# Performance work log

Measured on AMD Instinct MI355X. Metric: run time of the kernel, lower is better.

Reference implementation:

```python
import jax, jax.numpy as jnp
import numpy as np

B, N, H, NH = 8, 1024, 768, 12
AS = H // NH
SCALE = AS ** -0.5
NEG_SLOPE = 0.02  # LeakyReLU(0.02)
M = 256           # occurrence pairs per batch item


def _lin(k, out_d, in_d):
    k1, k2 = jax.random.split(k)
    w = jax.random.normal(k1, (out_d, in_d), jnp.float32) * (in_d ** -0.5)
    b = jax.random.normal(k2, (out_d,), jnp.float32) * 0.01
    return w, b


def setup_inputs():
    key = jax.random.key(0)
    ks = jax.random.split(key, 10)
    W_var, b_var = _lin(ks[0], H, H)
    W_sym, b_sym = _lin(ks[1], H, H)
    W_score, b_score = _lin(ks[2], 1, 2 * H)
    W_cross, b_cross = _lin(ks[3], 1, H)
    W_atom, b_atom = _lin(ks[4], H, 2 * H)
    W_q, b_q = _lin(ks[5], H, H)
    W_k, b_k = _lin(ks[6], H, H)
    W_v, b_v = _lin(ks[7], H, H)
    W_o, b_o = _lin(ks[8], H, H)
    x = jax.random.normal(ks[9], (B, N, H), jnp.float32)
    # predicates every 3rd node starting at 2 (no overlapping writes, i+1 < N)
    pp = np.zeros((B, N), np.int32)
    pp[:, 2:N - 2:3] = 1
    rng = np.random.default_rng(0)
    occ = np.stack([rng.permutation(N)[:2 * M].reshape(M, 2) for _ in range(B)]).astype(np.int32)
    return dict(
        x=x,
        atom_graph=jnp.zeros((B, N, N), jnp.float32),
        variable_graph=jnp.zeros((B, N, N), jnp.float32),
        W_var=W_var, b_var=b_var, W_sym=W_sym, b_sym=b_sym,
        W_score=W_score, b_score=b_score, W_cross=W_cross, b_cross=b_cross,
        W_atom=W_atom, b_atom=b_atom, W_q=W_q, b_q=b_q, W_k=W_k, b_k=b_k,
        W_v=W_v, b_v=b_v, W_o=W_o, b_o=b_o,
        predicate_pos=jnp.asarray(pp),
        variable_tags=jnp.zeros((B, N), jnp.int32),
        attention_mask=jnp.ones((B, N), jnp.int32),
        occurrence_list=jnp.asarray(occ),
    )


def reference(x, atom_graph, variable_graph,
              W_var, b_var, W_sym, b_sym, W_score, b_score, W_cross, b_cross,
              W_atom, b_atom, W_q, b_q, W_k, b_k, W_v, b_v, W_o, b_o,
              predicate_pos, variable_tags, attention_mask, occurrence_list):
    lrelu = lambda v: jax.nn.leaky_relu(v, NEG_SLOPE)
    idx = jnp.arange(N)
    pred = predicate_pos == 1                              # [B,N]
    pp_prev2 = jnp.roll(predicate_pos, 2, axis=1)          # pp[i-2]
    # branch: single-neighbor var (i==0 or pp[i-2]==1) vs averaged neighbors
    single = (idx[None, :] == 0) | ((idx[None, :] >= 2) & (pp_prev2 == 1))
    x_prev = jnp.roll(x, 1, axis=1)
    x_next = jnp.roll(x, -1, axis=1)
    var_in = jnp.where(single[..., None], x_next, (x_prev + x_next) * 0.5)
    var_feat = var_in @ W_var.T + b_var
    sym_feat = x @ W_sym.T + b_sym
    t = jnp.tanh(jnp.concatenate([var_feat, sym_feat], axis=-1))
    s = lrelu(t @ W_score.T + b_score)[..., 0]             # [B,N] edge scores
    # write masks: (i-1,i)/(i,i-1) for preds i>=1; (i,i+1)/(i+1,i) for i<=1 or double branch
    lower = pred & (idx[None, :] >= 1)
    upper = pred & ((idx[None, :] <= 1) | ~single)
    sl = jnp.where(lower, s, 0.0)
    su = jnp.where(upper, s, 0.0)
    im1 = jnp.clip(idx - 1, 0, N - 1)
    ip1 = jnp.clip(idx + 1, 0, N - 1)
    AG = atom_graph
    AG = AG.at[:, im1, idx].add(sl).at[:, idx, im1].add(sl)
    AG = AG.at[:, idx, ip1].add(su).at[:, ip1, idx].add(su)
    # variable (cross-atom occurrence) graph
    o0, o1 = occurrence_list[..., 0], occurrence_list[..., 1]
    barange = jnp.arange(B)[:, None]
    xm = (x[barange, o0] + x[barange, o1]) * 0.5           # [B,M,H]
    sc = lrelu(xm @ W_cross.T + b_cross)[..., 0]           # [B,M]
    VG = variable_graph.at[barange, o0, o1].add(sc).at[barange, o1, o0].add(sc)
    # multi-head attention with graph biases
    q = (x @ W_q.T + b_q).reshape(B, N, NH, AS).transpose(0, 2, 1, 3) * SCALE
    k = (x @ W_k.T + b_k).reshape(B, N, NH, AS).transpose(0, 2, 1, 3)
    v = (x @ W_v.T + b_v).reshape(B, N, NH, AS).transpose(0, 2, 1, 3)
    att = jnp.einsum('bhnd,bhmd->bhnm', q, k)
    AG = 0.2 * AG + 0.8 * (AG @ AG)
    VG2 = VG @ VG
    att = att + AG[:, None] + VG2[:, None]
    att = jax.nn.softmax(att, axis=-1)                     # dropout omitted (eval)
    y = jnp.einsum('bhnm,bhmd->bhnd', att, v).transpose(0, 2, 1, 3).reshape(B, N, H)
    y = y @ W_o.T + b_o
    # path embedding: weighted mean of per-predicate atom embeds (weight 2 or 3)
    y_prev = jnp.roll(y, 1, axis=1)
    y_next = jnp.roll(y, -1, axis=1)
    var_y = jnp.where(single[..., None], y_next, (y_prev + y_next) * 0.5)
    atom = jnp.concatenate([var_y, y], axis=-1) @ W_atom.T + b_atom  # [B,N,H]
    triple = upper & (idx[None, :] >= 1)
    w = jnp.where(pred, jnp.where(triple, 3.0, 2.0), 0.0)
    pm = (w[..., None] * atom).sum(axis=1) / w.sum(axis=1)[:, None]  # [B,H]
    return jnp.broadcast_to(pm[:, None, :], (B, N, H))
```

## Files before the change

### kernel.cpp

```cpp
#include <hip/hip_runtime.h>
#include <hip/hip_bf16.h>

#define BB 8
#define NN 1024
#define HH 768
#define NHD 12
#define ASZ 64
#define MM 256
#define QSCALE 0.125f
#define NSLOPE 0.02f
#define LOG2E 1.44269504f
#define PRMAX 384

typedef __attribute__((ext_vector_type(8))) short bf16x8;
typedef __attribute__((ext_vector_type(4))) float f32x4;

#define EXP2F(x) __builtin_amdgcn_exp2f(x)
#define RCPF(x)  __builtin_amdgcn_rcpf(x)

#define OFFB_QB    ((size_t)0)
#define OFFB_KB    ((size_t)12582912)
#define OFFB_VB    ((size_t)25165824)
#define OFFB_XB    ((size_t)37748736)
#define OFFB_WQB   ((size_t)50331648)
#define OFFB_WKB   ((size_t)51511296)
#define OFFB_WVB   ((size_t)52690944)
#define OFFB_WVAR  ((size_t)53870592)
#define OFFB_WSYM  ((size_t)55050240)
#define OFFB_SRAW  ((size_t)56229888)
#define OFFB_DIAG  ((size_t)56262656)
#define OFFB_BIAS4 ((size_t)56295424)
#define OFFB_PLIST ((size_t)56426496)
#define OFFB_PCNT  ((size_t)56459264)
#define OFFB_SUMW  ((size_t)56459296)
#define OFFB_ZZ    ((size_t)56459328)
#define OFFB_TV    ((size_t)56508480)
#define OFFB_PM    ((size_t)56557632)
#define OFFB_VROWS ((size_t)56582208)

__device__ __forceinline__ float lrelu(float v) { return v >= 0.f ? v : NSLOPE * v; }

__device__ __forceinline__ ushort f2bf(float f) {
  return (ushort)((__float_as_uint(f) + 0x8000u) >> 16);
}
__device__ __forceinline__ float bf2f(ushort u) {
  union { unsigned u; float f; } v; v.u = (unsigned)u << 16;
  return v.f;
}
__device__ __forceinline__ unsigned packbf2(float lo, float hi) {
  unsigned a = __float_as_uint(hi) + 0x8000u;
  unsigned b = __float_as_uint(lo) + 0x8000u;
  return __builtin_amdgcn_perm(a, b, 0x07060302u);
}
__device__ __forceinline__ float fast_tanh(float x) {
  float e = EXP2F(x * (2.f * LOG2E));
  return 1.f - 2.f * RCPF(e + 1.f);
}

__device__ __forceinline__ void coefs(const int* ppb, int j, float& c1, float& c2) {
  auto pred = [&](int tt) { return tt >= 0 && tt < NN && ppb[tt] == 1; };
  auto single = [&](int tt) { return tt == 0 || (tt >= 2 && ppb[tt - 2] == 1); };
  auto wgt = [&](int tt) {
    if (!pred(tt)) return 0.f;
    bool tri = (tt >= 1) && (tt <= 1 || !single(tt));
    return tri ? 3.f : 2.f;
  };
  float a = 0.f;
  if (pred(j + 1)) a += wgt(j + 1) * (single(j + 1) ? 0.f : 0.5f);
  if (j >= 1 && pred(j - 1)) a += wgt(j - 1) * (single(j - 1) ? 1.f : 0.5f);
  c1 = a;
  c2 = wgt(j);
}

__global__ void k_pred(const int* __restrict__ pp, int* __restrict__ plist,
                       int* __restrict__ pcnt, float* __restrict__ sumw,
                       float* __restrict__ sraw, float* __restrict__ diag,
                       float* __restrict__ zz) {
  int b = blockIdx.x;
  int lane = threadIdx.x;
  const int* ppb = pp + b * NN;
  int base = 0;
  float wacc = 0.f;
  for (int c = 0; c < NN; c += 64) {
    int i = c + lane;
    bool isp = ppb[i] == 1;
    unsigned long long mask = __ballot(isp);
    if (isp) {
      int pos = base + __popcll(mask & ((1ull << lane) - 1ull));
      plist[b * NN + pos] = i;
      bool sing = (i == 0) || (i >= 2 && ppb[i - 2] == 1);
      bool tri = (i >= 1) && (i <= 1 || !sing);
      wacc += tri ? 3.f : 2.f;
    }
    base += __popcll(mask);
  }
  for (int off = 32; off; off >>= 1) wacc += __shfl_xor(wacc, off);
  if (lane == 0) { pcnt[b] = base; sumw[b] = wacc; }
  for (int c = lane; c < NN; c += 64) { sraw[b * NN + c] = 0.f; diag[b * NN + c] = 0.f; }
  for (int c = lane; c < HH; c += 64) {
    zz[b * HH + c] = 0.f;
    zz[BB * HH + b * HH + c] = 0.f;
  }
}

#define NXQ (BB * NN * HH / 4)
#define WQ  (HH * HH / 4)
#define NCVT ((NXQ + 5 * WQ) / 256)
__global__ void k_cvtall(const float* __restrict__ x,
                         const float* __restrict__ s1, const float* __restrict__ s2,
                         const float* __restrict__ s3, const float* __restrict__ s4,
                         const float* __restrict__ s5,
                         ushort* __restrict__ dx,
                         ushort* __restrict__ d1, ushort* __restrict__ d2,
                         ushort* __restrict__ d3, ushort* __restrict__ d4,
                         ushort* __restrict__ d5,
                         const int* __restrict__ occ, const float* __restrict__ Wc,
                         const float* __restrict__ bc, float* __restrict__ diag) {
  if (blockIdx.x < NCVT) {
    int idx = blockIdx.x * 256 + threadIdx.x;
    const float* src; ushort* dst; int off;
    if (idx < NXQ) { src = x; dst = dx; off = idx; }
    else {
      int r = idx - NXQ;
      int z = r / WQ;
      off = r - z * WQ;
      src = z == 0 ? s1 : z == 1 ? s2 : z == 2 ? s3 : z == 3 ? s4 : s5;
      dst = z == 0 ? d1 : z == 1 ? d2 : z == 2 ? d3 : z == 3 ? d4 : d5;
    }
    float4 v = ((const float4*)src)[off];
    ushort4 o;
    o.x = f2bf(v.x); o.y = f2bf(v.y); o.z = f2bf(v.z); o.w = f2bf(v.w);
    ((ushort4*)dst)[off] = o;
  } else {
    int g = (blockIdx.x - NCVT) * 4 + (threadIdx.x >> 6);
    int lane = threadIdx.x & 63;
    int b = g >> 8, m = g & (MM - 1);
    int o0 = occ[(b * MM + m) * 2 + 0];
    int o1 = occ[(b * MM + m) * 2 + 1];
    const float* x0 = x + (size_t)(b * NN + o0) * HH;
    const float* x1 = x + (size_t)(b * NN + o1) * HH;
    float acc = 0.f;
    for (int d = lane; d < HH; d += 64) acc += 0.5f * (x0[d] + x1[d]) * Wc[d];
    for (int off = 32; off; off >>= 1) acc += __shfl_xor(acc, off);
    if (lane == 0) {
      float sc = lrelu(acc + bc[0]);
      float sq = sc * sc;
      diag[b * NN + o0] = sq;
      diag[b * NN + o1] = sq;
    }
  }
}

__global__ void k_gather(const ushort* __restrict__ xb, const int* __restrict__ pp,
                         const int* __restrict__ plist, const int* __restrict__ pcnt,
                         ushort* __restrict__ vrows) {
  int b = blockIdx.y;
  int j = blockIdx.x * 4 + (threadIdx.x >> 6);
  int lane = threadIdx.x & 63;
  if (j >= pcnt[b]) return;
  int i = plist[b * NN + j];
  bool sing = (i == 0) || (i >= 2 && pp[b * NN + i - 2] == 1);
  float wa = sing ? 0.f : 0.5f, wb = sing ? 1.f : 0.5f;
  const ushort* rp = xb + (size_t)(b * NN + ((i - 1) & (NN - 1))) * HH;
  const ushort* rn = xb + (size_t)(b * NN + ((i + 1) & (NN - 1))) * HH;
  ushort* dst = vrows + ((size_t)b * PRMAX + j) * HH;
#pragma unroll
  for (int it = 0; it < 3; ++it) {
    int d4 = lane + it * 64;
    ushort4 p4 = ((const ushort4*)rp)[d4];
    ushort4 n4 = ((const ushort4*)rn)[d4];
    ushort4 o;
    o.x = f2bf(wa * bf2f(p4.x) + wb * bf2f(n4.x));
    o.y = f2bf(wa * bf2f(p4.y) + wb * bf2f(n4.y));
    o.z = f2bf(wa * bf2f(p4.z) + wb * bf2f(n4.z));
    o.w = f2bf(wa * bf2f(p4.w) + wb * bf2f(n4.w));
    ((ushort4*)dst)[d4] = o;
  }
}

__global__ void k_bias(const int* __restrict__ pp, const float* __restrict__ s_raw,
                       const float* __restrict__ diag, const float* __restrict__ b_score,
                       float4* __restrict__ bias4) {
  int g = blockIdx.x * 256 + threadIdx.x;
  int b = g >> 10, r = g & (NN - 1);
  const int* ppb = pp + b * NN;
  int i = -1;
  if (ppb[r] == 1) i = r;
  else if (r + 1 < NN && ppb[r + 1] == 1) i = r + 1;
  else if (r >= 1 && ppb[r - 1] == 1) i = r - 1;
  float v0 = 0.f, v1 = 0.f, v2 = 0.f; int cw = r;
  if (i >= 1 && i + 1 < NN) {
    float s = lrelu(s_raw[b * NN + i] + b_score[0]);
    float s2 = s * s;
    cw = i - 1;
    if (i == r) { v0 = 0.2f * s; v1 = 1.6f * s2; v2 = 0.2f * s; }
    else       { v0 = 0.8f * s2; v1 = 0.2f * s; v2 = 0.8f * s2; }
  }
  int slot = r - cw;
  float d = diag[g];
  if (slot == 0) v0 += d; else if (slot == 1) v1 += d; else v2 += d;
  bias4[g] = make_float4(__int_as_float(cw), v0 * LOG2E, v1 * LOG2E, v2 * LOG2E);
}

#define GEMM_BLKS 1152
__global__ __launch_bounds__(256, 3) void k_mats(
    const ushort* __restrict__ X, const ushort* __restrict__ vrows,
    const int* __restrict__ plist, const int* __restrict__ pcnt,
    const ushort* __restrict__ Wvar, const ushort* __restrict__ Wsym,
    const float* __restrict__ bvar, const float* __restrict__ bsym,
    const float* __restrict__ wscore, float* __restrict__ s_raw,
    const ushort* __restrict__ W0, const ushort* __restrict__ W1, const ushort* __restrict__ W2,
    const float* __restrict__ b0, const float* __restrict__ b1, const float* __restrict__ b2,
    ushort* __restrict__ C0, ushort* __restrict__ C1, ushort* __restrict__ C2) {
  __shared__ ushort Sm[16384];
  __shared__ int pl[64];
  __shared__ float red[64];
  const int t = threadIdx.x;
  const int w = t >> 6, lane = t & 63, lg = lane >> 4, lm = lane & 15;
  const int r0 = t >> 3, c = t & 7;
  const int ssw = (c ^ (r0 & 7)) * 8;
  if (blockIdx.x < GEMM_BLKS) {
    const int z = blockIdx.x / 384;
    const int r = blockIdx.x % 384;
    const int m0 = (r & 63) * 128, n0 = (r >> 6) * 128;
    const ushort* W = z == 0 ? W0 : (z == 1 ? W1 : W2);
    const float* bias = z == 0 ? b0 : (z == 1 ? b1 : b2);
    ushort* C = z == 0 ? C0 : (z == 1 ? C1 : C2);
    const float alpha = z == 0 ? QSCALE * LOG2E : 1.f;
    ushort* As = Sm;
    ushort* Bs = Sm + 8192;
    const int wm = (w >> 1) * 64, wn = (w & 1) * 64;
    const ushort* Xp = X + (size_t)(m0 + r0) * HH + c * 8;
    const ushort* Wp = W + (size_t)(n0 + r0) * HH + c * 8;
    uint4 xa0 = *(const uint4*)Xp;
    uint4 xa1 = *(const uint4*)(Xp + (size_t)32 * HH);
    uint4 xa2 = *(const uint4*)(Xp + (size_t)64 * HH);
    uint4 xa3 = *(const uint4*)(Xp + (size_t)96 * HH);
    uint4 wb0 = *(const uint4*)Wp;
    uint4 wb1 = *(const uint4*)(Wp + (size_t)32 * HH);
    uint4 wb2 = *(const uint4*)(Wp + (size_t)64 * HH);
    uint4 wb3 = *(const uint4*)(Wp + (size_t)96 * HH);
    f32x4 acc[4][4] = {};
    for (int k0 = 0; k0 < HH; k0 += 64) {
      if (k0) __syncthreads();
      *(uint4*)&As[r0 * 64 + ssw] = xa0;
      *(uint4*)&As[(r0 + 32) * 64 + ssw] = xa1;
      *(uint4*)&As[(r0 + 64) * 64 + ssw] = xa2;
      *(uint4*)&As[(r0 + 96) * 64 + ssw] = xa3;
      *(uint4*)&Bs[r0 * 64 + ssw] = wb0;
      *(uint4*)&Bs[(r0 + 32) * 64 + ssw] = wb1;
      *(uint4*)&Bs[(r0 + 64) * 64 + ssw] = wb2;
      *(uint4*)&Bs[(r0 + 96) * 64 + ssw] = wb3;
      __syncthreads();
      if (k0 + 64 < HH) {
        Xp += 64; Wp += 64;
        xa0 = *(const uint4*)Xp;
        xa1 = *(const uint4*)(Xp + (size_t)32 * HH);
        xa2 = *(const uint4*)(Xp + (size_t)64 * HH);
        xa3 = *(const uint4*)(Xp + (size_t)96 * HH);
        wb0 = *(const uint4*)Wp;
        wb1 = *(const uint4*)(Wp + (size_t)32 * HH);
        wb2 = *(const uint4*)(Wp + (size_t)64 * HH);
        wb3 = *(const uint4*)(Wp + (size_t)96 * HH);
      }
      bf16x8 af[4][2], bfr[4][2];
#pragma unroll
      for (int mt = 0; mt < 4; ++mt)
#pragma unroll
        for (int kt = 0; kt < 2; ++kt) {
          int row = wm + mt * 16 + lm, ch = lg + kt * 4;
          af[mt][kt] = *(bf16x8*)&As[row * 64 + ((ch ^ (row & 7)) * 8)];
        }
#pragma unroll
      for (int nt = 0; nt < 4; ++nt)
#pragma unroll
        for (int kt = 0; kt < 2; ++kt) {
          int row = wn + nt * 16 + lm, ch = lg + kt * 4;
          bfr[nt][kt] = *(bf16x8*)&Bs[row * 64 + ((ch ^ (row & 7)) * 8)];
        }
#pragma unroll
      for (int mt = 0; mt < 4; ++mt)
#pragma unroll
        for (int nt = 0; nt < 4; ++nt)
#pragma unroll
          for (int kt = 0; kt < 2; ++kt)
            acc[mt][nt] = __builtin_amdgcn_mfma_f32_16x16x32_bf16(af[mt][kt], bfr[nt][kt], acc[mt][nt], 0, 0, 0);
    }
    if (z == 2) {
#pragma unroll
      for (int nt = 0; nt < 4; ++nt) {
        int col = n0 + wn + nt * 16 + lm;
        int hh = col >> 6, dd = col & 63;
        float bcol = bias[col];
#pragma unroll
        for (int mt = 0; mt < 4; ++mt) {
          int row0 = m0 + wm + mt * 16 + lg * 4;
          int bb2 = row0 >> 10, nr = row0 & (NN - 1);
          ushort4 o;
          o.x = f2bf(acc[mt][nt][0] + bcol);
          o.y = f2bf(acc[mt][nt][1] + bcol);
          o.z = f2bf(acc[mt][nt][2] + bcol);
          o.w = f2bf(acc[mt][nt][3] + bcol);
          *(ushort4*)(C + ((size_t)(bb2 * NHD + hh) * ASZ + dd) * NN + nr) = o;
        }
      }
    } else {
#pragma unroll
      for (int nt = 0; nt < 4; ++nt) {
        int col = n0 + wn + nt * 16 + lm;
        float bcol = bias[col];
#pragma unroll
        for (int mt = 0; mt < 4; ++mt)
#pragma unroll
          for (int rr = 0; rr < 4; ++rr) {
            int row = m0 + wm + mt * 16 + lg * 4 + rr;
            C[(size_t)row * HH + col] = f2bf((acc[mt][nt][rr] + bcol) * alpha);
          }
      }
    }
  } else {
    const int bid2 = blockIdx.x - GEMM_BLKS;
    const int b = bid2 / 72;
    const int rem = bid2 % 72;
    const int j0 = (rem / 12) * 64;
    const int n0g = (rem % 12) * 128;
    const int cnt = pcnt[b];
    if (j0 >= cnt) return;
    const bool symh = n0g >= HH;
    const int n0 = symh ? n0g - HH : n0g;
    const ushort* W = symh ? Wsym : Wvar;
    const float* bias = symh ? bsym : bvar;
    ushort* As = Sm;
    ushort* Bs = Sm + 4096;
    const int wm = (w >> 1) * 32, wn = (w & 1) * 64;
    if (t < 64) {
      int j = j0 + t;
      pl[t] = (j < cnt) ? plist[b * NN + j] : 2;
      red[t] = 0.f;
    }
    __syncthreads();
    const ushort* ap0; const ushort* ap1;
    if (symh) {
      const ushort* xbb = X + (size_t)b * NN * HH;
      ap0 = xbb + (size_t)pl[r0] * HH + c * 8;
      ap1 = xbb + (size_t)pl[r0 + 32] * HH + c * 8;
    } else {
      const ushort* vrb = vrows + ((size_t)b * PRMAX + j0) * HH;
      ap0 = vrb + (size_t)r0 * HH + c * 8;
      ap1 = vrb + (size_t)(r0 + 32) * HH + c * 8;
    }
    const ushort* bp = W + (size_t)(n0 + r0) * HH + c * 8;
    uint4 ar0 = *(const uint4*)ap0;
    uint4 ar1 = *(const uint4*)ap1;
    uint4 br0 = *(const uint4*)bp;
    uint4 br1 = *(const uint4*)(bp + (size_t)32 * HH);
    uint4 br2 = *(const uint4*)(bp + (size_t)64 * HH);
    uint4 br3 = *(const uint4*)(bp + (size_t)96 * HH);
    f32x4 acc[2][4] = {};
    for (int k0 = 0; k0 < HH; k0 += 64) {
      if (k0) __syncthreads();
      *(uint4*)&As[r0 * 64 + ssw] = ar0;
      *(uint4*)&As[(r0 + 32) * 64 + ssw] = ar1;
      *(uint4*)&Bs[r0 * 64 + ssw] = br0;
      *(uint4*)&Bs[(r0 + 32) * 64 + ssw] = br1;
      *(uint4*)&Bs[(r0 + 64) * 64 + ssw] = br2;
      *(uint4*)&Bs[(r0 + 96) * 64 + ssw] = br3;
      __syncthreads();
      if (k0 + 64 < HH) {
        ap0 += 64; ap1 += 64; bp += 64;
        ar0 = *(const uint4*)ap0;
        ar1 = *(const uint4*)ap1;
        br0 = *(const uint4*)bp;
        br1 = *(const uint4*)(bp + (size_t)32 * HH);
        br2 = *(const uint4*)(bp + (size_t)64 * HH);
        br3 = *(const uint4*)(bp + (size_t)96 * HH);
      }
      bf16x8 af[2][2], bfr[4][2];
#pragma unroll
      for (int mt = 0; mt < 2; ++mt)
#pragma unroll
        for (int kt = 0; kt < 2; ++kt) {
          int row = wm + mt * 16 + lm, ch = lg + kt * 4;
          af[mt][kt] = *(bf16x8*)&As[row * 64 + ((ch ^ (row & 7)) * 8)];
        }
#pragma unroll
      for (int nt = 0; nt < 4; ++nt)
#pragma unroll
        for (int kt = 0; kt < 2; ++kt) {
          int row = wn + nt * 16 + lm, ch = lg + kt * 4;
          bfr[nt][kt] = *(bf16x8*)&Bs[row * 64 + ((ch ^ (row & 7)) * 8)];
        }
#pragma unroll
      for (int mt = 0; mt < 2; ++mt)
#pragma unroll
        for (int nt = 0; nt < 4; ++nt)
#pragma unroll
          for (int kt = 0; kt < 2; ++kt)
            acc[mt][nt] = __builtin_amdgcn_mfma_f32_16x16x32_bf16(af[mt][kt], bfr[nt][kt], acc[mt][nt], 0, 0, 0);
    }
    float bcol[4], wcol[4];
#pragma unroll
    for (int nt = 0; nt < 4; ++nt) {
      int cl = wn + nt * 16 + lm;
      bcol[nt] = bias[n0 + cl];
      wcol[nt] = wscore[n0g + cl];
    }
#pragma unroll
    for (int mt = 0; mt < 2; ++mt)
#pragma unroll
      for (int rr = 0; rr < 4; ++rr) {
        float p = 0.f;
#pragma unroll
        for (int nt = 0; nt < 4; ++nt)
          p += fast_tanh(acc[mt][nt][rr] + bcol[nt]) * wcol[nt];
        p += __shfl_xor(p, 1); p += __shfl_xor(p, 2);
        p += __shfl_xor(p, 4); p += __shfl_xor(p, 8);
        if (lm == 0) atomicAdd(&red[wm + mt * 16 + lg * 4 + rr], p);
      }
    __syncthreads();
    if (t < 64) {
      int j2 = j0 + t;
      if (j2 < cnt) atomicAdd(&s_raw[b * NN + pl[t]], red[t]);
    }
  }
}

__global__ __launch_bounds__(256, 6) void k_attn2(
    const ushort* __restrict__ qg, const ushort* __restrict__ kg, const ushort* __restrict__ vtg,
    const float4* __restrict__ bias4, const int* __restrict__ pp, float* __restrict__ zz) {
  __shared__ ushort Ks[64 * 64];
  __shared__ ushort Vts[64 * 64];
  const int rb = blockIdx.y, h = blockIdx.x >> 3, b = blockIdx.x & 7;
  const int n0 = rb * 64;
  const int t = threadIdx.x, w = t >> 6, lane = t & 63, lg = lane >> 4, lm = lane & 15;
  const int qbase = n0 + w * 16;
  const ushort* qrow = qg + (size_t)(b * NN + qbase + lm) * HH + h * ASZ;
  bf16x8 qf[2];
  qf[0] = *(const bf16x8*)(qrow + lg * 8);
  qf[1] = *(const bf16x8*)(qrow + lg * 8 + 32);
  float4 bz = bias4[b * NN + qbase + lm];
  const int cwq = __float_as_int(bz.x);
  f32x4 suml = {0.f, 0.f, 0.f, 0.f};
  f32x4 y[4] = {};
  const ushort* kb = kg + (size_t)(b * NN) * HH + h * ASZ;
  const ushort* vtb = vtg + (size_t)(b * NHD + h) * ASZ * NN;
  const int srow = t >> 3, sc = t & 7;
  const int arow = (srow & 35) | ((srow & 4) << 2) | ((srow & 24) >> 1);
  const int kssw = (sc ^ (arow & 7)) * 8;
  const int vssw = (sc ^ (srow & 7)) * 8;
  const ushort* kptr = kb + (size_t)srow * HH + sc * 8;
  const ushort* vptr = vtb + (size_t)srow * NN + sc * 8;
  uint4 ka = *(const uint4*)kptr;
  uint4 kc = *(const uint4*)(kptr + (size_t)32 * HH);
  uint4 va = *(const uint4*)vptr;
  uint4 vb2 = *(const uint4*)(vptr + (size_t)32 * NN);
  for (int tile = 0; tile < 16; ++tile) {
    const int c0 = tile * 64;
    *(uint4*)&Ks[arow * 64 + kssw] = ka;
    *(uint4*)&Ks[(arow + 32) * 64 + kssw] = kc;
    *(uint4*)&Vts[srow * 64 + vssw] = va;
    *(uint4*)&Vts[(srow + 32) * 64 + vssw] = vb2;
    __syncthreads();
    if (tile < 15) {
      kptr += (size_t)64 * HH; vptr += 64;
      ka = *(const uint4*)kptr;
      kc = *(const uint4*)(kptr + (size_t)32 * HH);
      va = *(const uint4*)vptr;
      vb2 = *(const uint4*)(vptr + (size_t)32 * NN);
    }
    f32x4 s[4] = {};
    __builtin_amdgcn_s_setprio(1);
#pragma unroll
    for (int nt = 0; nt < 4; ++nt) {
      int krow = lm + nt * 16, sw = krow & 7;
#pragma unroll
      for (int kt = 0; kt < 2; ++kt) {
        bf16x8 kf = *(bf16x8*)&Ks[krow * 64 + (((lg + kt * 4) ^ sw) * 8)];
        s[nt] = __builtin_amdgcn_mfma_f32_16x16x32_bf16(kf, qf[kt], s[nt], 0, 0, 0);
      }
    }
    __builtin_amdgcn_s_setprio(0);
    if (c0 <= qbase + 17 && qbase <= c0 + 65) {
#pragma unroll
      for (int nt = 0; nt < 4; ++nt) {
        int kb2 = c0 + (nt >> 1) * 32 + lg * 8 + (nt & 1) * 4;
#pragma unroll
        for (int r = 0; r < 4; ++r) {
          int dd = kb2 + r - cwq;
          if (dd >= 0 && dd < 3) s[nt][r] += (dd == 0) ? bz.y : (dd == 1 ? bz.z : bz.w);
        }
      }
    }
#pragma unroll
    for (int nt = 0; nt < 4; ++nt)
#pragma unroll
      for (int e = 0; e < 4; ++e) {
        float p = EXP2F(s[nt][e]);
        s[nt][e] = p;
        suml[e] += p;
      }
    union { unsigned u[4]; bf16x8 v; } pk[2];
#pragma unroll
    for (int kt = 0; kt < 2; ++kt) {
      pk[kt].u[0] = packbf2(s[2 * kt][0], s[2 * kt][1]);
      pk[kt].u[1] = packbf2(s[2 * kt][2], s[2 * kt][3]);
      pk[kt].u[2] = packbf2(s[2 * kt + 1][0], s[2 * kt + 1][1]);
      pk[kt].u[3] = packbf2(s[2 * kt + 1][2], s[2 * kt + 1][3]);
    }
    __builtin_amdgcn_s_setprio(1);
#pragma unroll
    for (int nt = 0; nt < 4; ++nt) {
      int vrow = lm + nt * 16, sw = vrow & 7;
#pragma unroll
      for (int kt = 0; kt < 2; ++kt) {
        bf16x8 vf = *(bf16x8*)&Vts[vrow * 64 + (((lg + kt * 4) ^ sw) * 8)];
        y[nt] = __builtin_amdgcn_mfma_f32_16x16x32_bf16(pk[kt].v, vf, y[nt], 0, 0, 0);
      }
    }
    __builtin_amdgcn_s_setprio(0);
    __syncthreads();
  }
  float ts = (suml[0] + suml[1]) + (suml[2] + suml[3]);
  ts += __shfl_xor(ts, 16);
  ts += __shfl_xor(ts, 32);
  float invl = 1.f / ts;
  float invq[4], c1v[4], c2v[4];
#pragma unroll
  for (int r = 0; r < 4; ++r) {
    invq[r] = __shfl(invl, lg * 4 + r);
    coefs(pp + b * NN, qbase + lg * 4 + r, c1v[r], c2v[r]);
  }
  float a1[4], a2[4];
#pragma unroll
  for (int nt = 0; nt < 4; ++nt) {
    float u1 = 0.f, u2 = 0.f;
#pragma unroll
    for (int r = 0; r < 4; ++r) {
      float yv = y[nt][r] * invq[r];
      u1 += c1v[r] * yv;
      u2 += c2v[r] * yv;
    }
    u1 += __shfl_xor(u1, 16); u1 += __shfl_xor(u1, 32);
    u2 += __shfl_xor(u2, 16); u2 += __shfl_xor(u2, 32);
    a1[nt] = u1; a2[nt] = u2;
  }
  if (lg == 0) {
#pragma unroll
    for (int nt = 0; nt < 4; ++nt) {
      atomicAdd(&zz[b * HH + h * ASZ + nt * 16 + lm], a1[nt]);
      atomicAdd(&zz[BB * HH + b * HH + h * ASZ + nt * 16 + lm], a2[nt]);
    }
  }
}

__global__ void k_f1(const float* __restrict__ Wo, const float* __restrict__ bo,
                     const float* __restrict__ zz, const float* __restrict__ sumw,
                     float* __restrict__ tvec) {
  int b = blockIdx.y;
  int w = threadIdx.x >> 6, lane = threadIdx.x & 63;
  float inv = 1.f / sumw[b];
  const float* z1 = zz + b * HH;
  const float* z2 = zz + BB * HH + b * HH;
  float zr1[12], zr2[12];
#pragma unroll
  for (int m = 0; m < 12; ++m) { zr1[m] = z1[lane + 64 * m] * inv; zr2[m] = z2[lane + 64 * m] * inv; }
  for (int j = 0; j < 8; ++j) {
    int o = blockIdx.x * 32 + w * 8 + j;
    const float* wrow = Wo + (size_t)o * HH;
    float a1 = 0.f, a2 = 0.f;
#pragma unroll
    for (int m = 0; m < 12; ++m) { float wv = wrow[lane + 64 * m]; a1 += wv * zr1[m]; a2 += wv * zr2[m]; }
    for (int mask = 32; mask; mask >>= 1) { a1 += __shfl_xor(a1, mask); a2 += __shfl_xor(a2, mask); }
    if (lane == 0) { tvec[b * HH + o] = a1 + bo[o]; tvec[BB * HH + b * HH + o] = a2 + bo[o]; }
  }
}

__global__ void k_f2(const float* __restrict__ Wa, const float* __restrict__ ba,
                     const float* __restrict__ tvec, float* __restrict__ pm) {
  int b = blockIdx.y;
  int w = threadIdx.x >> 6, lane = threadIdx.x & 63;
  const float* t1 = tvec + b * HH;
  const float* t2 = tvec + BB * HH + b * HH;
  float r1[12], r2[12];
#pragma unroll
  for (int m = 0; m < 12; ++m) { r1[m] = t1[lane + 64 * m]; r2[m] = t2[lane + 64 * m]; }
  for (int j = 0; j < 8; ++j) {
    int o = blockIdx.x * 32 + w * 8 + j;
    const float* wrow = Wa + (size_t)o * (2 * HH);
    float a = 0.f;
#pragma unroll
    for (int m = 0; m < 12; ++m) a += wrow[lane + 64 * m] * r1[m];
#pragma unroll
    for (int m = 0; m < 12; ++m) a += wrow[HH + lane + 64 * m] * r2[m];
    for (int mask = 32; mask; mask >>= 1) a += __shfl_xor(a, mask);
    if (lane == 0) pm[b * HH + o] = a + ba[o];
  }
}

__global__ void k_bcast(const float* __restrict__ pm, float* __restrict__ out) {
  size_t g = (size_t)blockIdx.x * 256 + threadIdx.x;
  int b = (int)(g / ((size_t)NN * HH / 4));
  int hh4 = (int)(g % (HH / 4));
  float4 val = *(const float4*)(pm + b * HH + hh4 * 4);
  *(float4*)(out + g * 4) = val;
}

extern "C" void kernel_launch(void* const* d_in, const int* in_sizes, int n_in,
                              void* d_out, int out_size, void* d_ws, size_t ws_size,
                              hipStream_t stream) {
  (void)in_sizes; (void)n_in; (void)out_size; (void)ws_size;
  const float* x       = (const float*)d_in[0];
  const float* W_var   = (const float*)d_in[3];
  const float* b_var   = (const float*)d_in[4];
  const float* W_sym   = (const float*)d_in[5];
  const float* b_sym   = (const float*)d_in[6];
  const float* W_score = (const float*)d_in[7];
  const float* b_score = (const float*)d_in[8];
  const float* W_cross = (const float*)d_in[9];
  const float* b_cross = (const float*)d_in[10];
  const float* W_atom  = (const float*)d_in[11];
  const float* b_atom  = (const float*)d_in[12];
  const float* W_q     = (const float*)d_in[13];
  const float* b_q     = (const float*)d_in[14];
  const float* W_k     = (const float*)d_in[15];
  const float* b_k     = (const float*)d_in[16];
  const float* W_v     = (const float*)d_in[17];
  const float* b_v     = (const float*)d_in[18];
  const float* W_o     = (const float*)d_in[19];
  const float* b_o     = (const float*)d_in[20];
  const int*   pp      = (const int*)d_in[21];
  const int*   occ     = (const int*)d_in[24];
  float* out = (float*)d_out;
  char* wsb = (char*)d_ws;
  ushort* qb  = (ushort*)(wsb + OFFB_QB);
  ushort* kbf = (ushort*)(wsb + OFFB_KB);
  ushort* vtb = (ushort*)(wsb + OFFB_VB);
  ushort* xb  = (ushort*)(wsb + OFFB_XB);
  ushort* wqb = (ushort*)(wsb + OFFB_WQB);
  ushort* wkb = (ushort*)(wsb + OFFB_WKB);
  ushort* wvb = (ushort*)(wsb + OFFB_WVB);
  ushort* wvar = (ushort*)(wsb + OFFB_WVAR);
  ushort* wsym = (ushort*)(wsb + OFFB_WSYM);
  ushort* vrows = (ushort*)(wsb + OFFB_VROWS);
  float* sraw = (float*)(wsb + OFFB_SRAW);
  float* diag = (float*)(wsb + OFFB_DIAG);
  float4* bias4 = (float4*)(wsb + OFFB_BIAS4);
  int* plist = (int*)(wsb + OFFB_PLIST);
  int* pcnt  = (int*)(wsb + OFFB_PCNT);
  float* sumw = (float*)(wsb + OFFB_SUMW);
  float* zz   = (float*)(wsb + OFFB_ZZ);
  float* tv   = (float*)(wsb + OFFB_TV);
  float* pm   = (float*)(wsb + OFFB_PM);

  k_pred<<<BB, 64, 0, stream>>>(pp, plist, pcnt, sumw, sraw, diag, zz);
  k_cvtall<<<NCVT + BB * MM / 4, 256, 0, stream>>>(
      x, W_q, W_k, W_v, W_var, W_sym, xb, wqb, wkb, wvb, wvar, wsym,
      occ, W_cross, b_cross, diag);
  k_gather<<<dim3(PRMAX / 4, BB), 256, 0, stream>>>(xb, pp, plist, pcnt, vrows);
  k_mats<<<GEMM_BLKS + 576, 256, 0, stream>>>(
      xb, vrows, plist, pcnt, wvar, wsym, b_var, b_sym, W_score, sraw,
      wqb, wkb, wvb, b_q, b_k, b_v, qb, kbf, vtb);
  k_bias<<<BB * NN / 256, 256, 0, stream>>>(pp, sraw, diag, b_score, bias4);
  k_attn2<<<dim3(NHD * BB, NN / 64), 256, 0, stream>>>(qb, kbf, vtb, bias4, pp, zz);
  k_f1<<<dim3(24, BB), 256, 0, stream>>>(W_o, b_o, zz, sumw, tv);
  k_f2<<<dim3(24, BB), 256, 0, stream>>>(W_atom, b_atom, tv, pm);
  k_bcast<<<BB * NN * HH / 1024, 256, 0, stream>>>(pm, out);
}
```

Before: 153.7 us.

## Drop bf16 copy of x; convert on the fly in GEMM loads and fuse gather

The separate fp32→bf16 conversion of the whole x tensor is removed. The QKV and var/sym GEMMs now read fp32 x directly and pack it to bf16 as they stage into shared memory. The gather of neighbour rows is folded into the conversion kernel and reads fp32 x, which removes one launch. A block-index swizzle across the GEMM grid is also added. This saves a full write and read of the converted x, at the cost of doubling the global bytes the GEMM A-operand loads fetch and adding register pressure and conversion ALU work in the inner loop.

```diff
diff --git a/kernel.cpp b/kernel.cpp
--- a/kernel.cpp
+++ b/kernel.cpp
@@ -21,7 +21,6 @@
 #define OFFB_QB    ((size_t)0)
 #define OFFB_KB    ((size_t)12582912)
 #define OFFB_VB    ((size_t)25165824)
-#define OFFB_XB    ((size_t)37748736)
 #define OFFB_WQB   ((size_t)50331648)
 #define OFFB_WKB   ((size_t)51511296)
 #define OFFB_WVB   ((size_t)52690944)
@@ -42,10 +41,6 @@
 
 __device__ __forceinline__ ushort f2bf(float f) {
   return (ushort)((__float_as_uint(f) + 0x8000u) >> 16);
-}
-__device__ __forceinline__ float bf2f(ushort u) {
-  union { unsigned u; float f; } v; v.u = (unsigned)u << 16;
-  return v.f;
 }
 __device__ __forceinline__ unsigned packbf2(float lo, float hi) {
   unsigned a = __float_as_uint(hi) + 0x8000u;
@@ -103,36 +98,33 @@
   }
 }
 
-#define NXQ (BB * NN * HH / 4)
 #define WQ  (HH * HH / 4)
-#define NCVT ((NXQ + 5 * WQ) / 256)
+#define WCVTB (5 * WQ / 256)
+#define CROSSB (BB * MM / 4)
+#define GATB (PRMAX / 4 * BB)
 __global__ void k_cvtall(const float* __restrict__ x,
                          const float* __restrict__ s1, const float* __restrict__ s2,
                          const float* __restrict__ s3, const float* __restrict__ s4,
                          const float* __restrict__ s5,
-                         ushort* __restrict__ dx,
                          ushort* __restrict__ d1, ushort* __restrict__ d2,
                          ushort* __restrict__ d3, ushort* __restrict__ d4,
                          ushort* __restrict__ d5,
                          const int* __restrict__ occ, const float* __restrict__ Wc,
-                         const float* __restrict__ bc, float* __restrict__ diag) {
-  if (blockIdx.x < NCVT) {
+                         const float* __restrict__ bc, float* __restrict__ diag,
+                         const int* __restrict__ pp, const int* __restrict__ plist,
+                         const int* __restrict__ pcnt, ushort* __restrict__ vrows) {
+  if (blockIdx.x < WCVTB) {
     int idx = blockIdx.x * 256 + threadIdx.x;
-    const float* src; ushort* dst; int off;
-    if (idx < NXQ) { src = x; dst = dx; off = idx; }
-    else {
-      int r = idx - NXQ;
-      int z = r / WQ;
-      off = r - z * WQ;
-      src = z == 0 ? s1 : z == 1 ? s2 : z == 2 ? s3 : z == 3 ? s4 : s5;
-      dst = z == 0 ? d1 : z == 1 ? d2 : z == 2 ? d3 : z == 3 ? d4 : d5;
-    }
+    int z = idx / WQ;
+    int off = idx - z * WQ;
+    const float* src = z == 0 ? s1 : z == 1 ? s2 : z == 2 ? s3 : z == 3 ? s4 : s5;
+    ushort* dst = z == 0 ? d1 : z == 1 ? d2 : z == 2 ? d3 : z == 3 ? d4 : d5;
     float4 v = ((const float4*)src)[off];
     ushort4 o;
     o.x = f2bf(v.x); o.y = f2bf(v.y); o.z = f2bf(v.z); o.w = f2bf(v.w);
     ((ushort4*)dst)[off] = o;
-  } else {
-    int g = (blockIdx.x - NCVT) * 4 + (threadIdx.x >> 6);
+  } else if (blockIdx.x < WCVTB + CROSSB) {
+    int g = (blockIdx.x - WCVTB) * 4 + (threadIdx.x >> 6);
     int lane = threadIdx.x & 63;
     int b = g >> 8, m = g & (MM - 1);
     int o0 = occ[(b * MM + m) * 2 + 0];
@@ -148,33 +140,30 @@
       diag[b * NN + o0] = sq;
       diag[b * NN + o1] = sq;
     }
-  }
-}
-
-__global__ void k_gather(const ushort* __restrict__ xb, const int* __restrict__ pp,
-                         const int* __restrict__ plist, const int* __restrict__ pcnt,
-                         ushort* __restrict__ vrows) {
-  int b = blockIdx.y;
-  int j = blockIdx.x * 4 + (threadIdx.x >> 6);
-  int lane = threadIdx.x & 63;
-  if (j >= pcnt[b]) return;
-  int i = plist[b * NN + j];
-  bool sing = (i == 0) || (i >= 2 && pp[b * NN + i - 2] == 1);
-  float wa = sing ? 0.f : 0.5f, wb = sing ? 1.f : 0.5f;
-  const ushort* rp = xb + (size_t)(b * NN + ((i - 1) & (NN - 1))) * HH;
-  const ushort* rn = xb + (size_t)(b * NN + ((i + 1) & (NN - 1))) * HH;
-  ushort* dst = vrows + ((size_t)b * PRMAX + j) * HH;
-#pragma unroll
-  for (int it = 0; it < 3; ++it) {
-    int d4 = lane + it * 64;
-    ushort4 p4 = ((const ushort4*)rp)[d4];
-    ushort4 n4 = ((const ushort4*)rn)[d4];
-    ushort4 o;
-    o.x = f2bf(wa * bf2f(p4.x) + wb * bf2f(n4.x));
-    o.y = f2bf(wa * bf2f(p4.y) + wb * bf2f(n4.y));
-    o.z = f2bf(wa * bf2f(p4.z) + wb * bf2f(n4.z));
-    o.w = f2bf(wa * bf2f(p4.w) + wb * bf2f(n4.w));
-    ((ushort4*)dst)[d4] = o;
+  } else {
+    int g2 = blockIdx.x - (WCVTB + CROSSB);
+    int b = g2 / (PRMAX / 4);
+    int j = (g2 % (PRMAX / 4)) * 4 + (threadIdx.x >> 6);
+    int lane = threadIdx.x & 63;
+    if (j >= pcnt[b]) return;
+    int i = plist[b * NN + j];
+    bool sing = (i == 0) || (i >= 2 && pp[b * NN + i - 2] == 1);
+    float wa = sing ? 0.f : 0.5f, wb = sing ? 1.f : 0.5f;
+    const float* rp = x + (size_t)(b * NN + ((i - 1) & (NN - 1))) * HH;
+    const float* rn = x + (size_t)(b * NN + ((i + 1) & (NN - 1))) * HH;
+    ushort* dst = vrows + ((size_t)b * PRMAX + j) * HH;
+#pragma unroll
+    for (int it = 0; it < 3; ++it) {
+      int d4 = lane + it * 64;
+      float4 p4 = ((const float4*)rp)[d4];
+      float4 n4 = ((const float4*)rn)[d4];
+      ushort4 o;
+      o.x = f2bf(wa * p4.x + wb * n4.x);
+      o.y = f2bf(wa * p4.y + wb * n4.y);
+      o.z = f2bf(wa * p4.z + wb * n4.z);
+      o.w = f2bf(wa * p4.w + wb * n4.w);
+      ((ushort4*)dst)[d4] = o;
+    }
   }
 }
 
@@ -203,8 +192,9 @@
 }
 
 #define GEMM_BLKS 1152
+#define MATS_BLKS 1728
 __global__ __launch_bounds__(256, 3) void k_mats(
-    const ushort* __restrict__ X, const ushort* __restrict__ vrows,
+    const float* __restrict__ xf, const ushort* __restrict__ vrows,
     const int* __restrict__ plist, const int* __restrict__ pcnt,
     const ushort* __restrict__ Wvar, const ushort* __restrict__ Wsym,
     const float* __restrict__ bvar, const float* __restrict__ bsym,
@@ -215,13 +205,14 @@
   __shared__ ushort Sm[16384];
   __shared__ int pl[64];
   __shared__ float red[64];
+  const int bid = (blockIdx.x & 7) * (MATS_BLKS / 8) + (blockIdx.x >> 3);
   const int t = threadIdx.x;
   const int w = t >> 6, lane = t & 63, lg = lane >> 4, lm = lane & 15;
   const int r0 = t >> 3, c = t & 7;
   const int ssw = (c ^ (r0 & 7)) * 8;
-  if (blockIdx.x < GEMM_BLKS) {
-    const int z = blockIdx.x / 384;
-    const int r = blockIdx.x % 384;
+  if (bid < GEMM_BLKS) {
+    const int z = bid / 384;
+    const int r = bid % 384;
     const int m0 = (r & 63) * 128, n0 = (r >> 6) * 128;
     const ushort* W = z == 0 ? W0 : (z == 1 ? W1 : W2);
     const float* bias = z == 0 ? b0 : (z == 1 ? b1 : b2);
@@ -230,38 +221,36 @@
     ushort* As = Sm;
     ushort* Bs = Sm + 8192;
     const int wm = (w >> 1) * 64, wn = (w & 1) * 64;
-    const ushort* Xp = X + (size_t)(m0 + r0) * HH + c * 8;
+    const float* Xp = xf + (size_t)(m0 + r0) * HH + c * 8;
     const ushort* Wp = W + (size_t)(n0 + r0) * HH + c * 8;
-    uint4 xa0 = *(const uint4*)Xp;
-    uint4 xa1 = *(const uint4*)(Xp + (size_t)32 * HH);
-    uint4 xa2 = *(const uint4*)(Xp + (size_t)64 * HH);
-    uint4 xa3 = *(const uint4*)(Xp + (size_t)96 * HH);
-    uint4 wb0 = *(const uint4*)Wp;
-    uint4 wb1 = *(const uint4*)(Wp + (size_t)32 * HH);
-    uint4 wb2 = *(const uint4*)(Wp + (size_t)64 * HH);
-    uint4 wb3 = *(const uint4*)(Wp + (size_t)96 * HH);
+    float4 xaA[4], xaB[4];
+    uint4 wb[4];
+#pragma unroll
+    for (int i = 0; i < 4; ++i) {
+      xaA[i] = *(const float4*)(Xp + (size_t)(i * 32) * HH);
+      xaB[i] = *(const float4*)(Xp + (size_t)(i * 32) * HH + 4);
+      wb[i] = *(const uint4*)(Wp + (size_t)(i * 32) * HH);
+    }
     f32x4 acc[4][4] = {};
     for (int k0 = 0; k0 < HH; k0 += 64) {
       if (k0) __syncthreads();
-      *(uint4*)&As[r0 * 64 + ssw] = xa0;
-      *(uint4*)&As[(r0 + 32) * 64 + ssw] = xa1;
-      *(uint4*)&As[(r0 + 64) * 64 + ssw] = xa2;
-      *(uint4*)&As[(r0 + 96) * 64 + ssw] = xa3;
-      *(uint4*)&Bs[r0 * 64 + ssw] = wb0;
-      *(uint4*)&Bs[(r0 + 32) * 64 + ssw] = wb1;
-      *(uint4*)&Bs[(r0 + 64) * 64 + ssw] = wb2;
-      *(uint4*)&Bs[(r0 + 96) * 64 + ssw] = wb3;
+#pragma unroll
+      for (int i = 0; i < 4; ++i) {
+        uint4 u;
+        u.x = packbf2(xaA[i].x, xaA[i].y); u.y = packbf2(xaA[i].z, xaA[i].w);
+        u.z = packbf2(xaB[i].x, xaB[i].y); u.w = packbf2(xaB[i].z, xaB[i].w);
+        *(uint4*)&As[(r0 + i * 32) * 64 + ssw] = u;
+        *(uint4*)&Bs[(r0 + i * 32) * 64 + ssw] = wb[i];
+      }
       __syncthreads();
       if (k0 + 64 < HH) {
         Xp += 64; Wp += 64;
-        xa0 = *(const uint4*)Xp;
-        xa1 = *(const uint4*)(Xp + (size_t)32 * HH);
-        xa2 = *(const uint4*)(Xp + (size_t)64 * HH);
-        xa3 = *(const uint4*)(Xp + (size_t)96 * HH);
-        wb0 = *(const uint4*)Wp;
-        wb1 = *(const uint4*)(Wp + (size_t)32 * HH);
-        wb2 = *(const uint4*)(Wp + (size_t)64 * HH);
-        wb3 = *(const uint4*)(Wp + (size_t)96 * HH);
+#pragma unroll
+        for (int i = 0; i < 4; ++i) {
+          xaA[i] = *(const float4*)(Xp + (size_t)(i * 32) * HH);
+          xaB[i] = *(const float4*)(Xp + (size_t)(i * 32) * HH + 4);
+          wb[i] = *(const uint4*)(Wp + (size_t)(i * 32) * HH);
+        }
       }
       bf16x8 af[4][2], bfr[4][2];
 #pragma unroll
@@ -319,7 +308,7 @@
       }
     }
   } else {
-    const int bid2 = blockIdx.x - GEMM_BLKS;
+    const int bid2 = bid - GEMM_BLKS;
     const int b = bid2 / 72;
     const int rem = bid2 % 72;
     const int j0 = (rem / 12) * 64;
@@ -339,19 +328,28 @@
       red[t] = 0.f;
     }
     __syncthreads();
-    const ushort* ap0; const ushort* ap1;
+    const float* af0 = nullptr; const float* af1 = nullptr;
+    const ushort* ab0 = nullptr; const ushort* ab1 = nullptr;
     if (symh) {
-      const ushort* xbb = X + (size_t)b * NN * HH;
-      ap0 = xbb + (size_t)pl[r0] * HH + c * 8;
-      ap1 = xbb + (size_t)pl[r0 + 32] * HH + c * 8;
+      const float* xbb = xf + (size_t)b * NN * HH;
+      af0 = xbb + (size_t)pl[r0] * HH + c * 8;
+      af1 = xbb + (size_t)pl[r0 + 32] * HH + c * 8;
     } else {
       const ushort* vrb = vrows + ((size_t)b * PRMAX + j0) * HH;
-      ap0 = vrb + (size_t)r0 * HH + c * 8;
-      ap1 = vrb + (size_t)(r0 + 32) * HH + c * 8;
+      ab0 = vrb + (size_t)r0 * HH + c * 8;
+      ab1 = vrb + (size_t)(r0 + 32) * HH + c * 8;
     }
     const ushort* bp = W + (size_t)(n0 + r0) * HH + c * 8;
-    uint4 ar0 = *(const uint4*)ap0;
-    uint4 ar1 = *(const uint4*)ap1;
+    uint4 ar0, ar1;
+    if (symh) {
+      float4 a = *(const float4*)af0, b2 = *(const float4*)(af0 + 4);
+      ar0 = make_uint4(packbf2(a.x, a.y), packbf2(a.z, a.w), packbf2(b2.x, b2.y), packbf2(b2.z, b2.w));
+      a = *(const float4*)af1; b2 = *(const float4*)(af1 + 4);
+      ar1 = make_uint4(packbf2(a.x, a.y), packbf2(a.z, a.w), packbf2(b2.x, b2.y), packbf2(b2.z, b2.w));
+    } else {
+      ar0 = *(const uint4*)ab0;
+      ar1 = *(const uint4*)ab1;
+    }
     uint4 br0 = *(const uint4*)bp;
     uint4 br1 = *(const uint4*)(bp + (size_t)32 * HH);
     uint4 br2 = *(const uint4*)(bp + (size_t)64 * HH);
@@ -367,9 +365,18 @@
       *(uint4*)&Bs[(r0 + 96) * 64 + ssw] = br3;
       __syncthreads();
       if (k0 + 64 < HH) {
-        ap0 += 64; ap1 += 64; bp += 64;
-        ar0 = *(const uint4*)ap0;
-        ar1 = *(const uint4*)ap1;
+        bp += 64;
+        if (symh) {
+          af0 += 64; af1 += 64;
+          float4 a = *(const float4*)af0, b2 = *(const float4*)(af0 + 4);
+          ar0 = make_uint4(packbf2(a.x, a.y), packbf2(a.z, a.w), packbf2(b2.x, b2.y), packbf2(b2.z, b2.w));
+          a = *(const float4*)af1; b2 = *(const float4*)(af1 + 4);
+          ar1 = make_uint4(packbf2(a.x, a.y), packbf2(a.z, a.w), packbf2(b2.x, b2.y), packbf2(b2.z, b2.w));
+        } else {
+          ab0 += 64; ab1 += 64;
+          ar0 = *(const uint4*)ab0;
+          ar1 = *(const uint4*)ab1;
+        }
         br0 = *(const uint4*)bp;
         br1 = *(const uint4*)(bp + (size_t)32 * HH);
         br2 = *(const uint4*)(bp + (size_t)64 * HH);
@@ -635,7 +642,6 @@
   ushort* qb  = (ushort*)(wsb + OFFB_QB);
   ushort* kbf = (ushort*)(wsb + OFFB_KB);
   ushort* vtb = (ushort*)(wsb + OFFB_VB);
-  ushort* xb  = (ushort*)(wsb + OFFB_XB);
   ushort* wqb = (ushort*)(wsb + OFFB_WQB);
   ushort* wkb = (ushort*)(wsb + OFFB_WKB);
   ushort* wvb = (ushort*)(wsb + OFFB_WVB);
@@ -653,12 +659,11 @@
   float* pm   = (float*)(wsb + OFFB_PM);
 
   k_pred<<<BB, 64, 0, stream>>>(pp, plist, pcnt, sumw, sraw, diag, zz);
-  k_cvtall<<<NCVT + BB * MM / 4, 256, 0, stream>>>(
-      x, W_q, W_k, W_v, W_var, W_sym, xb, wqb, wkb, wvb, wvar, wsym,
-      occ, W_cross, b_cross, diag);
-  k_gather<<<dim3(PRMAX / 4, BB), 256, 0, stream>>>(xb, pp, plist, pcnt, vrows);
-  k_mats<<<GEMM_BLKS + 576, 256, 0, stream>>>(
-      xb, vrows, plist, pcnt, wvar, wsym, b_var, b_sym, W_score, sraw,
+  k_cvtall<<<WCVTB + CROSSB + GATB, 256, 0, stream>>>(
+      x, W_q, W_k, W_v, W_var, W_sym, wqb, wkb, wvb, wvar, wsym,
+      occ, W_cross, b_cross, diag, pp, plist, pcnt, vrows);
+  k_mats<<<MATS_BLKS, 256, 0, stream>>>(
+      x, vrows, plist, pcnt, wvar, wsym, b_var, b_sym, W_score, sraw,
       wqb, wkb, wvb, b_q, b_k, b_v, qb, kbf, vtb);
   k_bias<<<BB * NN / 256, 256, 0, stream>>>(pp, sraw, diag, b_score, bias4);
   k_attn2<<<dim3(NHD * BB, NN / 64), 256, 0, stream>>>(qb, kbf, vtb, bias4, pp, zz);
```

New measurement: 258.5 us. +68.2%, slower.
